# Performance work log

Measured on AMD Instinct MI355X. Metric: run time of the kernel, lower is better.

Reference implementation:

```python
import jax, jax.numpy as jnp
import numpy as np
from jax import lax

VOCAB = 12000
EMB = 512
RNN = 512
FEATS = 4096
SEQ_LEN = 15


def setup_inputs() -> dict:
    key = jax.random.key(0)
    ks = jax.random.split(key, 10)
    B = 1024
    s = 0.05
    return {
        "img_features": jax.random.normal(ks[0], (B, FEATS), jnp.float32),
        "W_feats": jax.random.normal(ks[1], (EMB, FEATS), jnp.float32) * s,
        "b_feats": jax.random.normal(ks[2], (EMB,), jnp.float32) * s,
        "W_ih": jax.random.normal(ks[3], (4 * RNN, EMB), jnp.float32) * s,
        "W_hh": jax.random.normal(ks[4], (4 * RNN, RNN), jnp.float32) * s,
        "b_ih": jax.random.normal(ks[5], (4 * RNN,), jnp.float32) * s,
        "b_hh": jax.random.normal(ks[6], (4 * RNN,), jnp.float32) * s,
        "emb": jax.random.normal(ks[7], (VOCAB, EMB), jnp.float32) * s,
        "W_out": jax.random.normal(ks[8], (VOCAB - 2, RNN), jnp.float32) * s,
        "b_out": jax.random.normal(ks[9], (VOCAB - 2,), jnp.float32) * s,
    }


def reference(img_features, W_feats, b_feats, W_ih, W_hh, b_ih, b_hh, emb, W_out, b_out):
    B = img_features.shape[0]

    def lstm_cell(x, h, c):
        # torch.nn.LSTMCell: gates ordered i, f, g, o
        gates = x @ W_ih.T + b_ih + h @ W_hh.T + b_hh
        i, f, g, o = jnp.split(gates, 4, axis=1)
        c_new = jax.nn.sigmoid(f) * c + jax.nn.sigmoid(i) * jnp.tanh(g)
        h_new = jax.nn.sigmoid(o) * jnp.tanh(c_new)
        return h_new, c_new

    # image feature embedding + ReLU, then prime the LSTM with it
    img_vec = jax.nn.relu(img_features @ W_feats.T + b_feats)  # [B, 512]
    h = jnp.zeros((B, RNN), img_features.dtype)
    c = jnp.zeros((B, RNN), img_features.dtype)
    h, c = lstm_cell(img_vec, h, c)

    def step(carry, _):
        h, c, words = carry
        x = emb[words]                     # [B, 512] embedding lookup
        h, c = lstm_cell(x, h, c)
        logits = h @ W_out.T + b_out       # [B, VOCAB-2]
        idx = jnp.argmax(logits, axis=1).astype(jnp.int32)
        return (h, c, idx + 2), idx

    words0 = jnp.ones((B,), jnp.int32)  # START token = 1
    _, seq = lax.scan(step, (h, c, words0), None, length=SEQ_LEN)
    return seq.T  # [B, SEQ_LEN] greedy-decoded token ids
```

## Files before the change

kernel.cpp:

```cpp
#include <hip/hip_runtime.h>
#include <stdint.h>

#define BATCH  1024
#define SEQLEN 15
#define NGATE  2048
#define NVOCAB 11998
#define FEATS  4096

typedef __attribute__((ext_vector_type(8)))  short  s8v;
typedef __attribute__((ext_vector_type(16))) float  f32x16;
typedef __attribute__((ext_vector_type(8)))  unsigned short us8;

__device__ __forceinline__ unsigned short f2bf(float f) {
    unsigned u = __float_as_uint(f);
    u += 0x7FFFu + ((u >> 16) & 1u);
    return (unsigned short)(u >> 16);
}
__device__ __forceinline__ float bf2f(unsigned short h) {
    return __uint_as_float(((unsigned)h) << 16);
}
struct bfpair { unsigned short hi, lo; };
__device__ __forceinline__ bfpair split2v(float v) {
    bfpair r;
    r.hi = f2bf(v);
    r.lo = f2bf(v - bf2f(r.hi));
    return r;
}
__device__ __forceinline__ void split8(const float* __restrict__ s, us8& vh, us8& vl) {
    #pragma unroll
    for (int e = 0; e < 8; ++e) {
        bfpair q = split2v(s[e]);
        vh[e] = q.hi; vl[e] = q.lo;
    }
}

__device__ __forceinline__ void async_cp16(const void* g, void* l) {
    __builtin_amdgcn_global_load_lds(
        (const __attribute__((address_space(1))) unsigned int*)g,
        (__attribute__((address_space(3))) unsigned int*)l, 16, 0, 0);
}

__global__ void prep_wcat_blk(const float* __restrict__ W_ih, const float* __restrict__ W_hh,
                              const float* __restrict__ b_ih, const float* __restrict__ b_hh,
                              unsigned short* __restrict__ hi, unsigned short* __restrict__ lo,
                              float* __restrict__ bsum) {
    int idx = blockIdx.x * 256 + threadIdx.x;
    int kc = idx >> 11, row = idx & 2047;
    int k = kc << 3;
    const float* src = (k < 512) ? (W_ih + (size_t)row * 512 + k)
                                 : (W_hh + (size_t)row * 512 + (k - 512));
    us8 vh, vl; split8(src, vh, vl);
    *(us8*)(hi + (size_t)idx * 8) = vh;
    *(us8*)(lo + (size_t)idx * 8) = vl;
    if (idx < NGATE) bsum[idx] = b_ih[idx] + b_hh[idx];
}

__global__ void prep_blk(const float* __restrict__ src,
                         unsigned short* __restrict__ hi, unsigned short* __restrict__ lo,
                         int R, int K) {
    int row = blockIdx.x * 256 + threadIdx.x;
    if (row >= R) return;
    int kc = blockIdx.y;
    us8 vh, vl; split8(src + (size_t)row * K + (kc << 3), vh, vl);
    size_t o = ((size_t)kc * R + row) * 8;
    *(us8*)(hi + o) = vh;
    *(us8*)(lo + o) = vl;
}

template<int MODE>
__device__ __forceinline__ void mfma_blk_body(
    const unsigned short* __restrict__ Ahi, const unsigned short* __restrict__ Alo, int aRows,
    const unsigned short* __restrict__ Bhi, const unsigned short* __restrict__ Blo, int bRows,
    const float* __restrict__ bias,
    float* __restrict__ C, int ldc,
    unsigned long long* __restrict__ packed,
    int N, int K, size_t akstride, size_t bkstride, size_t czstride)
{
    __shared__ short smem[4 * 4 * 128 * 8];
    short* sAhi = smem;
    short* sAlo = smem + 4 * 128 * 8;
    short* sBhi = smem + 2 * 4 * 128 * 8;
    short* sBlo = smem + 3 * 4 * 128 * 8;

    const int kz = blockIdx.z;
    Ahi += kz * akstride;  Alo += kz * akstride;
    Bhi += kz * bkstride;  Blo += kz * bkstride;
    if (MODE == 3) C += kz * czstride;

    const int tid  = threadIdx.x;
    const int lane = tid & 63, wave = tid >> 6;
    const int wr = (wave & 1) * 64, wc = (wave >> 1) * 64;
    const int col = lane & 31, kh = lane >> 5;
    const int bm = blockIdx.y * 128, bn = blockIdx.x * 128;

    f32x16 acc[2][2] = {};

    for (int k0 = 0; k0 < K; k0 += 32) {
        const int kc0 = k0 >> 3;
        __syncthreads();
        #pragma unroll
        for (int p = 0; p < 2; ++p) {
            int s    = p * 4 + wave;
            int kc_l = s >> 1, rh = s & 1;
            int rl   = rh * 64 + lane;
            int lo_  = (kc_l * 128 + rh * 64) * 8;
            size_t ga = ((size_t)(kc0 + kc_l) * aRows + (bm + rl)) * 8;
            async_cp16(Ahi + ga, sAhi + lo_);
            async_cp16(Alo + ga, sAlo + lo_);
            int brow = bn + rl; if (brow > N - 1) brow = N - 1;
            size_t gb = ((size_t)(kc0 + kc_l) * bRows + brow) * 8;
            async_cp16(Bhi + gb, sBhi + lo_);
            async_cp16(Blo + gb, sBlo + lo_);
        }
        __syncthreads();

        #pragma unroll
        for (int st = 0; st < 2; ++st) {
            int off = (2 * st + kh) * 128 * 8;
            s8v ah0 = *(const s8v*)(sAhi + off + (wr + col) * 8);
            s8v ah1 = *(const s8v*)(sAhi + off + (wr + 32 + col) * 8);
            s8v al0 = *(const s8v*)(sAlo + off + (wr + col) * 8);
            s8v al1 = *(const s8v*)(sAlo + off + (wr + 32 + col) * 8);
            s8v bh0 = *(const s8v*)(sBhi + off + (wc + col) * 8);
            s8v bh1 = *(const s8v*)(sBhi + off + (wc + 32 + col) * 8);
            s8v bl0 = *(const s8v*)(sBlo + off + (wc + col) * 8);
            s8v bl1 = *(const s8v*)(sBlo + off + (wc + 32 + col) * 8);

            acc[0][0] = __builtin_amdgcn_mfma_f32_32x32x16_bf16(ah0, bh0, acc[0][0], 0, 0, 0);
            acc[0][1] = __builtin_amdgcn_mfma_f32_32x32x16_bf16(ah0, bh1, acc[0][1], 0, 0, 0);
            acc[1][0] = __builtin_amdgcn_mfma_f32_32x32x16_bf16(ah1, bh0, acc[1][0], 0, 0, 0);
            acc[1][1] = __builtin_amdgcn_mfma_f32_32x32x16_bf16(ah1, bh1, acc[1][1], 0, 0, 0);
            acc[0][0] = __builtin_amdgcn_mfma_f32_32x32x16_bf16(ah0, bl0, acc[0][0], 0, 0, 0);
            acc[0][1] = __builtin_amdgcn_mfma_f32_32x32x16_bf16(ah0, bl1, acc[0][1], 0, 0, 0);
            acc[1][0] = __builtin_amdgcn_mfma_f32_32x32x16_bf16(ah1, bl0, acc[1][0], 0, 0, 0);
            acc[1][1] = __builtin_amdgcn_mfma_f32_32x32x16_bf16(ah1, bl1, acc[1][1], 0, 0, 0);
            acc[0][0] = __builtin_amdgcn_mfma_f32_32x32x16_bf16(al0, bh0, acc[0][0], 0, 0, 0);
            acc[0][1] = __builtin_amdgcn_mfma_f32_32x32x16_bf16(al0, bh1, acc[0][1], 0, 0, 0);
            acc[1][0] = __builtin_amdgcn_mfma_f32_32x32x16_bf16(al1, bh0, acc[1][0], 0, 0, 0);
            acc[1][1] = __builtin_amdgcn_mfma_f32_32x32x16_bf16(al1, bh1, acc[1][1], 0, 0, 0);
        }
    }

    if (MODE == 3) {
        #pragma unroll
        for (int i = 0; i < 2; ++i)
            #pragma unroll
            for (int rg = 0; rg < 4; ++rg)
                #pragma unroll
                for (int rr = 0; rr < 4; ++rr) {
                    int reg = rg * 4 + rr;
                    int m = bm + wr + i * 32 + rr + rg * 8 + kh * 4;
                    #pragma unroll
                    for (int j = 0; j < 2; ++j) {
                        int n = bn + wc + j * 32 + col;
                        if (n < N) C[(size_t)m * ldc + n] = acc[i][j][reg];
                    }
                }
    } else {
        #pragma unroll
        for (int i = 0; i < 2; ++i)
            #pragma unroll
            for (int rg = 0; rg < 4; ++rg)
                #pragma unroll
                for (int rr = 0; rr < 4; ++rr) {
                    int reg = rg * 4 + rr;
                    int m = bm + wr + i * 32 + rr + rg * 8 + kh * 4;
                    unsigned long long best = 0ull;
                    #pragma unroll
                    for (int j = 0; j < 2; ++j) {
                        int n = bn + wc + j * 32 + col;
                        if (n < N) {
                            float v = acc[i][j][reg] + bias[n];
                            unsigned int u   = __float_as_uint(v);
                            unsigned int key = (u & 0x80000000u) ? ~u : (u | 0x80000000u);
                            unsigned long long pk =
                                ((unsigned long long)key << 32) |
                                (unsigned long long)(0xFFFFFFFFu - (unsigned)n);
                            best = (pk > best) ? pk : best;
                        }
                    }
                    #pragma unroll
                    for (int sdist = 1; sdist < 32; sdist <<= 1) {
                        unsigned long long o = __shfl_xor(best, sdist, 64);
                        best = (o > best) ? o : best;
                    }
                    if (col == 0) atomicMax(&packed[m], best);
                }
    }
}

__global__ __launch_bounds__(256) void k_gemm_feats(
    const unsigned short* Ahi, const unsigned short* Alo, int aRows,
    const unsigned short* Bhi, const unsigned short* Blo, int bRows,
    float* C, int ldc, int N, int K, size_t aks, size_t bks, size_t czs) {
    mfma_blk_body<3>(Ahi, Alo, aRows, Bhi, Blo, bRows, nullptr, C, ldc, nullptr, N, K, aks, bks, czs);
}
__global__ __launch_bounds__(256) void k_gemm_gates(
    const unsigned short* Ahi, const unsigned short* Alo, int aRows,
    const unsigned short* Bhi, const unsigned short* Blo, int bRows,
    float* C, int ldc, int N, int K, size_t aks, size_t bks, size_t czs) {
    mfma_blk_body<3>(Ahi, Alo, aRows, Bhi, Blo, bRows, nullptr, C, ldc, nullptr, N, K, aks, bks, czs);
}
__global__ __launch_bounds__(256) void k_logits_argmax(
    const unsigned short* Ahi, const unsigned short* Alo, int aRows,
    const unsigned short* Bhi, const unsigned short* Blo, int bRows,
    const float* bias, unsigned long long* packed, int N, int K) {
    mfma_blk_body<2>(Ahi, Alo, aRows, Bhi, Blo, bRows, bias, nullptr, 0, packed, N, K, 0, 0, 0);
}

__global__ void feats_reduce8(const float* __restrict__ part, const float* __restrict__ bias,
                              unsigned short* __restrict__ hi, unsigned short* __restrict__ lo) {
    int idx = blockIdx.x * 256 + threadIdx.x;
    int b = idx >> 6, kc = idx & 63;
    int n = kc << 3;
    float v[8];
    #pragma unroll
    for (int e = 0; e < 8; ++e) v[e] = bias[n + e];
    #pragma unroll
    for (int z = 0; z < 8; ++z) {
        const float* s = part + (size_t)z * 1024 * 512 + (size_t)b * 512 + n;
        #pragma unroll
        for (int e = 0; e < 8; ++e) v[e] += s[e];
    }
    us8 vh, vl;
    #pragma unroll
    for (int e = 0; e < 8; ++e) {
        bfpair q = split2v(fmaxf(v[e], 0.f));
        vh[e] = q.hi; vl[e] = q.lo;
    }
    size_t o = ((size_t)kc * 1024 + b) * 8;
    *(us8*)(hi + o) = vh;
    *(us8*)(lo + o) = vl;
}

template<bool PRIME>
__global__ void lstm_pw_blk(const float* __restrict__ g0, const float* __restrict__ g1,
                            const float* __restrict__ bsum, float* __restrict__ cbuf,
                            unsigned short* __restrict__ xh_hi, unsigned short* __restrict__ xh_lo,
                            unsigned long long* __restrict__ packed) {
    int idx = blockIdx.x * 256 + threadIdx.x;
    int b = idx >> 6, j8 = idx & 63;
    int j = j8 << 3;
    const float* g = g0 + (size_t)b * NGATE;
    float v[4][8];
    #pragma unroll
    for (int gt = 0; gt < 4; ++gt) {
        const float* s = g + gt * 512 + j;
        const float* bs = bsum + gt * 512 + j;
        #pragma unroll
        for (int e = 0; e < 8; ++e) v[gt][e] = s[e] + bs[e];
    }
    if (g1) {
        const float* h2 = g1 + (size_t)b * NGATE;
        #pragma unroll
        for (int gt = 0; gt < 4; ++gt) {
            const float* s = h2 + gt * 512 + j;
            #pragma unroll
            for (int e = 0; e < 8; ++e) v[gt][e] += s[e];
        }
    }
    float* cb = cbuf + (size_t)b * 512 + j;
    us8 vh, vl;
    #pragma unroll
    for (int e = 0; e < 8; ++e) {
        float si = 1.f / (1.f + expf(-v[0][e]));
        float sf = 1.f / (1.f + expf(-v[1][e]));
        float tg = tanhf(v[2][e]);
        float so = 1.f / (1.f + expf(-v[3][e]));
        float cn = PRIME ? (si * tg) : (sf * cb[e] + si * tg);
        cb[e] = cn;
        bfpair q = split2v(so * tanhf(cn));
        vh[e] = q.hi; vl[e] = q.lo;
    }
    size_t o = ((size_t)(64 + j8) * 1024 + b) * 8;
    *(us8*)(xh_hi + o) = vh;
    *(us8*)(xh_lo + o) = vl;
    if (j8 == 0) packed[b] = 0ull;
}

template<int FIRST>
__global__ void gather_blk(const float* __restrict__ emb,
                           const unsigned long long* __restrict__ packed,
                           unsigned short* __restrict__ xh_hi, unsigned short* __restrict__ xh_lo,
                           int* __restrict__ out, int t) {
    int idx = blockIdx.x * 256 + threadIdx.x;
    int b = idx >> 6, kc = idx & 63;
    int word;
    if (FIRST) {
        word = 1;
    } else {
        unsigned long long p = packed[b];
        int id = (int)(0xFFFFFFFFu - (unsigned)(p & 0xFFFFFFFFull));
        word = id + 2;
        if (kc == 0) out[b * SEQLEN + (t - 1)] = id;
    }
    us8 vh, vl; split8(emb + (size_t)word * 512 + (kc << 3), vh, vl);
    size_t o = ((size_t)kc * 1024 + b) * 8;
    *(us8*)(xh_hi + o) = vh;
    *(us8*)(xh_lo + o) = vl;
}

__global__ void final_out(const unsigned long long* __restrict__ packed, int* __restrict__ out) {
    int b = blockIdx.x * 256 + threadIdx.x;
    if (b < BATCH) {
        unsigned long long p = packed[b];
        out[b * SEQLEN + (SEQLEN - 1)] = (int)(0xFFFFFFFFu - (unsigned)(p & 0xFFFFFFFFull));
    }
}

extern "C" void kernel_launch(void* const* d_in, const int* in_sizes, int n_in,
                              void* d_out, int out_size, void* d_ws, size_t ws_size,
                              hipStream_t stream) {
    const float* img     = (const float*)d_in[0];
    const float* W_feats = (const float*)d_in[1];
    const float* b_feats = (const float*)d_in[2];
    const float* W_ih    = (const float*)d_in[3];
    const float* W_hh    = (const float*)d_in[4];
    const float* b_ih    = (const float*)d_in[5];
    const float* b_hh    = (const float*)d_in[6];
    const float* emb     = (const float*)d_in[7];
    const float* W_out   = (const float*)d_in[8];
    const float* b_out   = (const float*)d_in[9];
    int* out = (int*)d_out;

    const size_t WCAT_H = (size_t)128 * 2048 * 8;
    const size_t WOUT_H = (size_t)64 * NVOCAB * 8;
    const size_t XH_H   = (size_t)128 * 1024 * 8;
    const size_t IMGV_H = (size_t)64 * 1024 * 8;

    char* p = (char*)d_ws;
    unsigned short* wcat_hi = (unsigned short*)p;  p += WCAT_H * 2;
    unsigned short* wcat_lo = (unsigned short*)p;  p += WCAT_H * 2;
    unsigned short* wout_hi = (unsigned short*)p;  p += WOUT_H * 2;
    unsigned short* wout_lo = (unsigned short*)p;  p += WOUT_H * 2;
    unsigned short* xh_hi   = (unsigned short*)p;  p += XH_H * 2;
    unsigned short* xh_lo   = (unsigned short*)p;  p += XH_H * 2;
    unsigned short* imgv_hi = (unsigned short*)p;  p += IMGV_H * 2;
    unsigned short* imgv_lo = (unsigned short*)p;  p += IMGV_H * 2;
    float* cbuf             = (float*)p;           p += (size_t)1024 * 512 * 4;
    float* bsum             = (float*)p;           p += (size_t)NGATE * 4;
    unsigned long long* packed = (unsigned long long*)p;  p += (size_t)1024 * 8;
    float* gates0           = (float*)p;           p += (size_t)1024 * NGATE * 4;
    float* gates1           = (float*)p;           p += (size_t)1024 * NGATE * 4;
    unsigned short* imgb_hi = wout_hi;
    unsigned short* imgb_lo = imgb_hi + (size_t)512 * 1024 * 8;
    unsigned short* wfb_hi  = imgb_lo + (size_t)512 * 1024 * 8;
    unsigned short* wfb_lo  = wfb_hi  + (size_t)512 * 512 * 8;
    float* partials = gates0;

    prep_wcat_blk<<<1024, 256, 0, stream>>>(W_ih, W_hh, b_ih, b_hh, wcat_hi, wcat_lo, bsum);
    prep_blk<<<dim3(4, 512), 256, 0, stream>>>(img,     imgb_hi, imgb_lo, 1024, FEATS);
    prep_blk<<<dim3(2, 512), 256, 0, stream>>>(W_feats, wfb_hi,  wfb_lo,  512,  FEATS);

    k_gemm_feats<<<dim3(4, 8, 8), 256, 0, stream>>>(
        imgb_hi, imgb_lo, 1024, wfb_hi, wfb_lo, 512,
        partials, 512, 512, 512,
        (size_t)64 * 1024 * 8, (size_t)64 * 512 * 8, (size_t)1024 * 512);
    feats_reduce8<<<256, 256, 0, stream>>>(partials, b_feats, imgv_hi, imgv_lo);

    prep_blk<<<dim3(47, 64), 256, 0, stream>>>(W_out, wout_hi, wout_lo, NVOCAB, 512);

    k_gemm_gates<<<dim3(16, 8, 1), 256, 0, stream>>>(
        imgv_hi, imgv_lo, 1024, wcat_hi, wcat_lo, 2048,
        gates0, NGATE, NGATE, 512, 0, 0, 0);
    lstm_pw_blk<true><<<256, 256, 0, stream>>>(gates0, nullptr, bsum, cbuf, xh_hi, xh_lo, packed);

    for (int t = 0; t < SEQLEN; ++t) {
        if (t == 0) gather_blk<1><<<256, 256, 0, stream>>>(emb, packed, xh_hi, xh_lo, out, t);
        else        gather_blk<0><<<256, 256, 0, stream>>>(emb, packed, xh_hi, xh_lo, out, t);

        k_gemm_gates<<<dim3(16, 8, 2), 256, 0, stream>>>(
            xh_hi, xh_lo, 1024, wcat_hi, wcat_lo, 2048,
            gates0, NGATE, NGATE, 512,
            (size_t)64 * 1024 * 8, (size_t)64 * 2048 * 8, (size_t)1024 * NGATE);
        lstm_pw_blk<false><<<256, 256, 0, stream>>>(gates0, gates1, bsum, cbuf, xh_hi, xh_lo, packed);

        k_logits_argmax<<<dim3(94, 8, 1), 256, 0, stream>>>(
            xh_hi + (size_t)64 * 1024 * 8, xh_lo + (size_t)64 * 1024 * 8, 1024,
            wout_hi, wout_lo, NVOCAB, b_out, packed, NVOCAB, 512);
    }
    final_out<<<4, 256, 0, stream>>>(packed, out);
}
```

Baseline: 1.845 ms.

## Fuse embedding gather into gates GEMM, double-buffer LDS, swizzle logits blocks by XCD

```diff
diff --git a/kernel.cpp b/kernel.cpp
--- a/kernel.cpp
+++ b/kernel.cpp
@@ -33,6 +33,7 @@
         vh[e] = q.hi; vl[e] = q.lo;
     }
 }
+__device__ __forceinline__ int imin(int a, int b) { return a < b ? a : b; }
 
 __device__ __forceinline__ void async_cp16(const void* g, void* l) {
     __builtin_amdgcn_global_load_lds(
@@ -67,78 +68,121 @@
     *(us8*)(lo + o) = vl;
 }
 
-template<int MODE>
-__device__ __forceinline__ void mfma_blk_body(
+template<int MODE, int AEMB, int FIRST>
+__device__ __forceinline__ void gemm_body(
     const unsigned short* __restrict__ Ahi, const unsigned short* __restrict__ Alo, int aRows,
     const unsigned short* __restrict__ Bhi, const unsigned short* __restrict__ Blo, int bRows,
+    const float* __restrict__ emb, const unsigned long long* __restrict__ packedR,
     const float* __restrict__ bias,
     float* __restrict__ C, int ldc,
     unsigned long long* __restrict__ packed,
-    int N, int K, size_t akstride, size_t bkstride, size_t czstride)
+    int K, size_t akstride, size_t bkstride, size_t czstride,
+    int bm, int bn)
 {
-    __shared__ short smem[4 * 4 * 128 * 8];
-    short* sAhi = smem;
-    short* sAlo = smem + 4 * 128 * 8;
-    short* sBhi = smem + 2 * 4 * 128 * 8;
-    short* sBlo = smem + 3 * 4 * 128 * 8;
-
-    const int kz = blockIdx.z;
-    Ahi += kz * akstride;  Alo += kz * akstride;
-    Bhi += kz * bkstride;  Blo += kz * bkstride;
-    if (MODE == 3) C += kz * czstride;
-
-    const int tid  = threadIdx.x;
+    __shared__ short smem[2 * 8192];
+    const int tid = threadIdx.x;
     const int lane = tid & 63, wave = tid >> 6;
     const int wr = (wave & 1) * 64, wc = (wave >> 1) * 64;
     const int col = lane & 31, kh = lane >> 5;
-    const int bm = blockIdx.y * 128, bn = blockIdx.x * 128;
-
+
+    const int kz = blockIdx.z;
+    Bhi += (size_t)kz * bkstride;  Blo += (size_t)kz * bkstride;
+    const bool embp = AEMB && (kz == 0);
+    if (!embp) { Ahi += (size_t)kz * akstride; Alo += (size_t)kz * akstride; }
+    if (MODE == 3) C += (size_t)kz * czstride;
+
+    const float* embrow = nullptr;
+    int arow = 0, akcp = 0;
+    if (embp) {
+        arow = tid >> 1; akcp = tid & 1;
+        int w = 1;
+        if (!FIRST) {
+            unsigned long long p = packedR[bm + arow];
+            w = (int)(0xFFFFFFFFu - (unsigned)(p & 0xFFFFFFFFull)) + 2;
+        }
+        embrow = emb + (size_t)w * 512 + akcp * 8;
+    }
+
+    const int nIter = K >> 4;
     f32x16 acc[2][2] = {};
 
-    for (int k0 = 0; k0 < K; k0 += 32) {
-        const int kc0 = k0 >> 3;
+    auto stage = [&](int it) {
+        const int kcg = it * 2;
+        short* base = smem + (it & 1) * 8192;
+        if (!embp) {
+            const unsigned short* gsrc = (wave == 0) ? Ahi : (wave == 1) ? Alo
+                                       : (wave == 2) ? Bhi : Blo;
+            const int rows = (wave < 2) ? aRows : bRows;
+            const bool isB = (wave >= 2);
+            short* abase = base + wave * 2048;
+            #pragma unroll
+            for (int p = 0; p < 4; ++p) {
+                int kc_l = p >> 1, rh = p & 1;
+                int rl = rh * 64 + lane;
+                int grow = isB ? imin(bn + rl, rows - 1) : (bm + rl);
+                size_t g = ((size_t)(kcg + kc_l) * rows + grow) * 8;
+                async_cp16(gsrc + g, abase + (kc_l * 128 + rh * 64) * 8);
+            }
+        } else {
+            #pragma unroll
+            for (int p = 0; p < 2; ++p) {
+                int s = wave * 2 + p;
+                int arr = s >> 2, kc_l = (s >> 1) & 1, rh = s & 1;
+                const unsigned short* gsrc = arr ? Blo : Bhi;
+                int rl = rh * 64 + lane;
+                int grow = imin(bn + rl, bRows - 1);
+                size_t g = ((size_t)(kcg + kc_l) * bRows + grow) * 8;
+                async_cp16(gsrc + g, base + (2 + arr) * 2048 + (kc_l * 128 + rh * 64) * 8);
+            }
+            float4 f0 = *(const float4*)(embrow + kcg * 8);
+            float4 f1 = *(const float4*)(embrow + kcg * 8 + 4);
+            float fb[8] = {f0.x, f0.y, f0.z, f0.w, f1.x, f1.y, f1.z, f1.w};
+            us8 vh, vl;
+            #pragma unroll
+            for (int e = 0; e < 8; ++e) {
+                bfpair q = split2v(fb[e]);
+                vh[e] = q.hi; vl[e] = q.lo;
+            }
+            short* d = base + (akcp * 128 + arow) * 8;
+            *(us8*)(d) = vh;
+            *(us8*)(d + 2048) = vl;
+        }
+    };
+
+    auto consume = [&](int it) {
+        short* base = smem + (it & 1) * 8192;
+        const int off = kh * 1024;
+        const short* pAhi = base + off;
+        const short* pAlo = base + 2048 + off;
+        const short* pBhi = base + 4096 + off;
+        const short* pBlo = base + 6144 + off;
+        s8v ah0 = *(const s8v*)(pAhi + (wr + col) * 8);
+        s8v ah1 = *(const s8v*)(pAhi + (wr + 32 + col) * 8);
+        s8v al0 = *(const s8v*)(pAlo + (wr + col) * 8);
+        s8v al1 = *(const s8v*)(pAlo + (wr + 32 + col) * 8);
+        s8v bh0 = *(const s8v*)(pBhi + (wc + col) * 8);
+        s8v bh1 = *(const s8v*)(pBhi + (wc + 32 + col) * 8);
+        s8v bl0 = *(const s8v*)(pBlo + (wc + col) * 8);
+        s8v bl1 = *(const s8v*)(pBlo + (wc + 32 + col) * 8);
+        acc[0][0] = __builtin_amdgcn_mfma_f32_32x32x16_bf16(ah0, bh0, acc[0][0], 0, 0, 0);
+        acc[0][1] = __builtin_amdgcn_mfma_f32_32x32x16_bf16(ah0, bh1, acc[0][1], 0, 0, 0);
+        acc[1][0] = __builtin_amdgcn_mfma_f32_32x32x16_bf16(ah1, bh0, acc[1][0], 0, 0, 0);
+        acc[1][1] = __builtin_amdgcn_mfma_f32_32x32x16_bf16(ah1, bh1, acc[1][1], 0, 0, 0);
+        acc[0][0] = __builtin_amdgcn_mfma_f32_32x32x16_bf16(ah0, bl0, acc[0][0], 0, 0, 0);
+        acc[0][1] = __builtin_amdgcn_mfma_f32_32x32x16_bf16(ah0, bl1, acc[0][1], 0, 0, 0);
+        acc[1][0] = __builtin_amdgcn_mfma_f32_32x32x16_bf16(ah1, bl0, acc[1][0], 0, 0, 0);
+        acc[1][1] = __builtin_amdgcn_mfma_f32_32x32x16_bf16(ah1, bl1, acc[1][1], 0, 0, 0);
+        acc[0][0] = __builtin_amdgcn_mfma_f32_32x32x16_bf16(al0, bh0, acc[0][0], 0, 0, 0);
+        acc[0][1] = __builtin_amdgcn_mfma_f32_32x32x16_bf16(al0, bh1, acc[0][1], 0, 0, 0);
+        acc[1][0] = __builtin_amdgcn_mfma_f32_32x32x16_bf16(al1, bh0, acc[1][0], 0, 0, 0);
+        acc[1][1] = __builtin_amdgcn_mfma_f32_32x32x16_bf16(al1, bh1, acc[1][1], 0, 0, 0);
+    };
+
+    stage(0);
+    for (int it = 0; it < nIter; ++it) {
         __syncthreads();
-        #pragma unroll
-        for (int p = 0; p < 2; ++p) {
-            int s    = p * 4 + wave;
-            int kc_l = s >> 1, rh = s & 1;
-            int rl   = rh * 64 + lane;
-            int lo_  = (kc_l * 128 + rh * 64) * 8;
-            size_t ga = ((size_t)(kc0 + kc_l) * aRows + (bm + rl)) * 8;
-            async_cp16(Ahi + ga, sAhi + lo_);
-            async_cp16(Alo + ga, sAlo + lo_);
-            int brow = bn + rl; if (brow > N - 1) brow = N - 1;
-            size_t gb = ((size_t)(kc0 + kc_l) * bRows + brow) * 8;
-            async_cp16(Bhi + gb, sBhi + lo_);
-            async_cp16(Blo + gb, sBlo + lo_);
-        }
-        __syncthreads();
-
-        #pragma unroll
-        for (int st = 0; st < 2; ++st) {
-            int off = (2 * st + kh) * 128 * 8;
-            s8v ah0 = *(const s8v*)(sAhi + off + (wr + col) * 8);
-            s8v ah1 = *(const s8v*)(sAhi + off + (wr + 32 + col) * 8);
-            s8v al0 = *(const s8v*)(sAlo + off + (wr + col) * 8);
-            s8v al1 = *(const s8v*)(sAlo + off + (wr + 32 + col) * 8);
-            s8v bh0 = *(const s8v*)(sBhi + off + (wc + col) * 8);
-            s8v bh1 = *(const s8v*)(sBhi + off + (wc + 32 + col) * 8);
-            s8v bl0 = *(const s8v*)(sBlo + off + (wc + col) * 8);
-            s8v bl1 = *(const s8v*)(sBlo + off + (wc + 32 + col) * 8);
-
-            acc[0][0] = __builtin_amdgcn_mfma_f32_32x32x16_bf16(ah0, bh0, acc[0][0], 0, 0, 0);
-            acc[0][1] = __builtin_amdgcn_mfma_f32_32x32x16_bf16(ah0, bh1, acc[0][1], 0, 0, 0);
-            acc[1][0] = __builtin_amdgcn_mfma_f32_32x32x16_bf16(ah1, bh0, acc[1][0], 0, 0, 0);
-            acc[1][1] = __builtin_amdgcn_mfma_f32_32x32x16_bf16(ah1, bh1, acc[1][1], 0, 0, 0);
-            acc[0][0] = __builtin_amdgcn_mfma_f32_32x32x16_bf16(ah0, bl0, acc[0][0], 0, 0, 0);
-            acc[0][1] = __builtin_amdgcn_mfma_f32_32x32x16_bf16(ah0, bl1, acc[0][1], 0, 0, 0);
-            acc[1][0] = __builtin_amdgcn_mfma_f32_32x32x16_bf16(ah1, bl0, acc[1][0], 0, 0, 0);
-            acc[1][1] = __builtin_amdgcn_mfma_f32_32x32x16_bf16(ah1, bl1, acc[1][1], 0, 0, 0);
-            acc[0][0] = __builtin_amdgcn_mfma_f32_32x32x16_bf16(al0, bh0, acc[0][0], 0, 0, 0);
-            acc[0][1] = __builtin_amdgcn_mfma_f32_32x32x16_bf16(al0, bh1, acc[0][1], 0, 0, 0);
-            acc[1][0] = __builtin_amdgcn_mfma_f32_32x32x16_bf16(al1, bh0, acc[1][0], 0, 0, 0);
-            acc[1][1] = __builtin_amdgcn_mfma_f32_32x32x16_bf16(al1, bh1, acc[1][1], 0, 0, 0);
-        }
+        if (it + 1 < nIter) stage(it + 1);
+        consume(it);
     }
 
     if (MODE == 3) {
@@ -153,7 +197,7 @@
                     #pragma unroll
                     for (int j = 0; j < 2; ++j) {
                         int n = bn + wc + j * 32 + col;
-                        if (n < N) C[(size_t)m * ldc + n] = acc[i][j][reg];
+                        if (n < bRows) C[(size_t)m * ldc + n] = acc[i][j][reg];
                     }
                 }
     } else {
@@ -169,7 +213,7 @@
                     #pragma unroll
                     for (int j = 0; j < 2; ++j) {
                         int n = bn + wc + j * 32 + col;
-                        if (n < N) {
+                        if (n < bRows) {
                             float v = acc[i][j][reg] + bias[n];
                             unsigned int u   = __float_as_uint(v);
                             unsigned int key = (u & 0x80000000u) ? ~u : (u | 0x80000000u);
@@ -189,23 +233,36 @@
     }
 }
 
-__global__ __launch_bounds__(256) void k_gemm_feats(
+__global__ __launch_bounds__(256) void k_mm(
     const unsigned short* Ahi, const unsigned short* Alo, int aRows,
     const unsigned short* Bhi, const unsigned short* Blo, int bRows,
-    float* C, int ldc, int N, int K, size_t aks, size_t bks, size_t czs) {
-    mfma_blk_body<3>(Ahi, Alo, aRows, Bhi, Blo, bRows, nullptr, C, ldc, nullptr, N, K, aks, bks, czs);
-}
-__global__ __launch_bounds__(256) void k_gemm_gates(
-    const unsigned short* Ahi, const unsigned short* Alo, int aRows,
-    const unsigned short* Bhi, const unsigned short* Blo, int bRows,
-    float* C, int ldc, int N, int K, size_t aks, size_t bks, size_t czs) {
-    mfma_blk_body<3>(Ahi, Alo, aRows, Bhi, Blo, bRows, nullptr, C, ldc, nullptr, N, K, aks, bks, czs);
+    float* C, int ldc, int K, size_t aks, size_t bks, size_t czs) {
+    gemm_body<3, 0, 0>(Ahi, Alo, aRows, Bhi, Blo, bRows, nullptr, nullptr, nullptr,
+                       C, ldc, nullptr, K, aks, bks, czs,
+                       blockIdx.y * 128, blockIdx.x * 128);
+}
+template<int FIRST>
+__global__ __launch_bounds__(256) void k_gates_f(
+    const unsigned short* h_hi, const unsigned short* h_lo,
+    const unsigned short* wcat_hi, const unsigned short* wcat_lo,
+    const float* emb, const unsigned long long* packedR,
+    float* C) {
+    gemm_body<3, 1, FIRST>(h_hi, h_lo, 1024, wcat_hi, wcat_lo, NGATE,
+                           emb, packedR, nullptr, C, NGATE, nullptr,
+                           512, 0, (size_t)64 * NGATE * 8, (size_t)1024 * NGATE,
+                           blockIdx.y * 128, blockIdx.x * 128);
 }
 __global__ __launch_bounds__(256) void k_logits_argmax(
-    const unsigned short* Ahi, const unsigned short* Alo, int aRows,
-    const unsigned short* Bhi, const unsigned short* Blo, int bRows,
-    const float* bias, unsigned long long* packed, int N, int K) {
-    mfma_blk_body<2>(Ahi, Alo, aRows, Bhi, Blo, bRows, bias, nullptr, 0, packed, N, K, 0, 0, 0);
+    const unsigned short* h_hi, const unsigned short* h_lo,
+    const unsigned short* wout_hi, const unsigned short* wout_lo,
+    const float* bias, unsigned long long* packed) {
+    int id = blockIdx.x;
+    int xcd = id & 7, slot = id >> 3;
+    int bn_t = xcd * 12 + (slot % 12);
+    int bm_t = slot / 12;
+    gemm_body<2, 0, 0>(h_hi, h_lo, 1024, wout_hi, wout_lo, NVOCAB,
+                       nullptr, nullptr, bias, nullptr, 0, packed,
+                       512, 0, 0, 0, bm_t * 128, bn_t * 128);
 }
 
 __global__ void feats_reduce8(const float* __restrict__ part, const float* __restrict__ bias,
@@ -236,8 +293,9 @@
 template<bool PRIME>
 __global__ void lstm_pw_blk(const float* __restrict__ g0, const float* __restrict__ g1,
                             const float* __restrict__ bsum, float* __restrict__ cbuf,
-                            unsigned short* __restrict__ xh_hi, unsigned short* __restrict__ xh_lo,
-                            unsigned long long* __restrict__ packed) {
+                            unsigned short* __restrict__ h_hi, unsigned short* __restrict__ h_lo,
+                            unsigned long long* __restrict__ packed,
+                            int* __restrict__ out, int t) {
     int idx = blockIdx.x * 256 + threadIdx.x;
     int b = idx >> 6, j8 = idx & 63;
     int j = j8 << 3;
@@ -272,32 +330,16 @@
         bfpair q = split2v(so * tanhf(cn));
         vh[e] = q.hi; vl[e] = q.lo;
     }
-    size_t o = ((size_t)(64 + j8) * 1024 + b) * 8;
-    *(us8*)(xh_hi + o) = vh;
-    *(us8*)(xh_lo + o) = vl;
-    if (j8 == 0) packed[b] = 0ull;
-}
-
-template<int FIRST>
-__global__ void gather_blk(const float* __restrict__ emb,
-                           const unsigned long long* __restrict__ packed,
-                           unsigned short* __restrict__ xh_hi, unsigned short* __restrict__ xh_lo,
-                           int* __restrict__ out, int t) {
-    int idx = blockIdx.x * 256 + threadIdx.x;
-    int b = idx >> 6, kc = idx & 63;
-    int word;
-    if (FIRST) {
-        word = 1;
-    } else {
-        unsigned long long p = packed[b];
-        int id = (int)(0xFFFFFFFFu - (unsigned)(p & 0xFFFFFFFFull));
-        word = id + 2;
-        if (kc == 0) out[b * SEQLEN + (t - 1)] = id;
-    }
-    us8 vh, vl; split8(emb + (size_t)word * 512 + (kc << 3), vh, vl);
-    size_t o = ((size_t)kc * 1024 + b) * 8;
-    *(us8*)(xh_hi + o) = vh;
-    *(us8*)(xh_lo + o) = vl;
+    size_t o = ((size_t)j8 * 1024 + b) * 8;
+    *(us8*)(h_hi + o) = vh;
+    *(us8*)(h_lo + o) = vl;
+    if (j8 == 0) {
+        if (!PRIME && t > 0) {
+            unsigned long long p = packed[b];
+            out[b * SEQLEN + (t - 1)] = (int)(0xFFFFFFFFu - (unsigned)(p & 0xFFFFFFFFull));
+        }
+        packed[b] = 0ull;
+    }
 }
 
 __global__ void final_out(const unsigned long long* __restrict__ packed, int* __restrict__ out) {
@@ -325,7 +367,7 @@
 
     const size_t WCAT_H = (size_t)128 * 2048 * 8;
     const size_t WOUT_H = (size_t)64 * NVOCAB * 8;
-    const size_t XH_H   = (size_t)128 * 1024 * 8;
+    const size_t H_H    = (size_t)64 * 1024 * 8;
     const size_t IMGV_H = (size_t)64 * 1024 * 8;
 
     char* p = (char*)d_ws;
@@ -333,8 +375,8 @@
     unsigned short* wcat_lo = (unsigned short*)p;  p += WCAT_H * 2;
     unsigned short* wout_hi = (unsigned short*)p;  p += WOUT_H * 2;
     unsigned short* wout_lo = (unsigned short*)p;  p += WOUT_H * 2;
-    unsigned short* xh_hi   = (unsigned short*)p;  p += XH_H * 2;
-    unsigned short* xh_lo   = (unsigned short*)p;  p += XH_H * 2;
+    unsigned short* h_hi    = (unsigned short*)p;  p += H_H * 2;
+    unsigned short* h_lo    = (unsigned short*)p;  p += H_H * 2;
     unsigned short* imgv_hi = (unsigned short*)p;  p += IMGV_H * 2;
     unsigned short* imgv_lo = (unsigned short*)p;  p += IMGV_H * 2;
     float* cbuf             = (float*)p;           p += (size_t)1024 * 512 * 4;
@@ -352,32 +394,30 @@
     prep_blk<<<dim3(4, 512), 256, 0, stream>>>(img,     imgb_hi, imgb_lo, 1024, FEATS);
     prep_blk<<<dim3(2, 512), 256, 0, stream>>>(W_feats, wfb_hi,  wfb_lo,  512,  FEATS);
 
-    k_gemm_feats<<<dim3(4, 8, 8), 256, 0, stream>>>(
+    k_mm<<<dim3(4, 8, 8), 256, 0, stream>>>(
         imgb_hi, imgb_lo, 1024, wfb_hi, wfb_lo, 512,
-        partials, 512, 512, 512,
+        partials, 512, 512,
         (size_t)64 * 1024 * 8, (size_t)64 * 512 * 8, (size_t)1024 * 512);
     feats_reduce8<<<256, 256, 0, stream>>>(partials, b_feats, imgv_hi, imgv_lo);
 
     prep_blk<<<dim3(47, 64), 256, 0, stream>>>(W_out, wout_hi, wout_lo, NVOCAB, 512);
 
-    k_gemm_gates<<<dim3(16, 8, 1), 256, 0, stream>>>(
+    k_mm<<<dim3(16, 8, 1), 256, 0, stream>>>(
         imgv_hi, imgv_lo, 1024, wcat_hi, wcat_lo, 2048,
-        gates0, NGATE, NGATE, 512, 0, 0, 0);
-    lstm_pw_blk<true><<<256, 256, 0, stream>>>(gates0, nullptr, bsum, cbuf, xh_hi, xh_lo, packed);
+        gates0, NGATE, 512, 0, 0, 0);
+    lstm_pw_blk<true><<<256, 256, 0, stream>>>(gates0, nullptr, bsum, cbuf,
+                                               h_hi, h_lo, packed, out, 0);
 
     for (int t = 0; t < SEQLEN; ++t) {
-        if (t == 0) gather_blk<1><<<256, 256, 0, stream>>>(emb, packed, xh_hi, xh_lo, out, t);
-        else        gather_blk<0><<<256, 256, 0, stream>>>(emb, packed, xh_hi, xh_lo, out, t);
-
-        k_gemm_gates<<<dim3(16, 8, 2), 256, 0, stream>>>(
-            xh_hi, xh_lo, 1024, wcat_hi, wcat_lo, 2048,
-            gates0, NGATE, NGATE, 512,
-            (size_t)64 * 1024 * 8, (size_t)64 * 2048 * 8, (size_t)1024 * NGATE);
-        lstm_pw_blk<false><<<256, 256, 0, stream>>>(gates0, gates1, bsum, cbuf, xh_hi, xh_lo, packed);
-
-        k_logits_argmax<<<dim3(94, 8, 1), 256, 0, stream>>>(
-            xh_hi + (size_t)64 * 1024 * 8, xh_lo + (size_t)64 * 1024 * 8, 1024,
-            wout_hi, wout_lo, NVOCAB, b_out, packed, NVOCAB, 512);
+        if (t == 0)
+            k_gates_f<1><<<dim3(16, 8, 2), 256, 0, stream>>>(
+                h_hi, h_lo, wcat_hi, wcat_lo, emb, packed, gates0);
+        else
+            k_gates_f<0><<<dim3(16, 8, 2), 256, 0, stream>>>(
+                h_hi, h_lo, wcat_hi, wcat_lo, emb, packed, gates0);
+        lstm_pw_blk<false><<<256, 256, 0, stream>>>(gates0, gates1, bsum, cbuf,
+                                                    h_hi, h_lo, packed, out, t);
+        k_logits_argmax<<<768, 256, 0, stream>>>(h_hi, h_lo, wout_hi, wout_lo, b_out, packed);
     }
     final_out<<<4, 256, 0, stream>>>(packed, out);
 }
```

Result: slower. 1.948 ms (+5.6%).

## Replace LDS-staged MFMA GEMMs with direct-register flat kernels and drop gates split-K

Applied to the files above, without the earlier changes.

```diff
diff --git a/kernel.cpp b/kernel.cpp
--- a/kernel.cpp
+++ b/kernel.cpp
@@ -32,12 +32,6 @@
         bfpair q = split2v(s[e]);
         vh[e] = q.hi; vl[e] = q.lo;
     }
-}
-
-__device__ __forceinline__ void async_cp16(const void* g, void* l) {
-    __builtin_amdgcn_global_load_lds(
-        (const __attribute__((address_space(1))) unsigned int*)g,
-        (__attribute__((address_space(3))) unsigned int*)l, 16, 0, 0);
 }
 
 __global__ void prep_wcat_blk(const float* __restrict__ W_ih, const float* __restrict__ W_hh,
@@ -67,77 +61,59 @@
     *(us8*)(lo + o) = vl;
 }
 
-template<int MODE>
-__device__ __forceinline__ void mfma_blk_body(
+template<int MODE, int NF, int K>
+__device__ __forceinline__ void flat_body(
     const unsigned short* __restrict__ Ahi, const unsigned short* __restrict__ Alo, int aRows,
     const unsigned short* __restrict__ Bhi, const unsigned short* __restrict__ Blo, int bRows,
-    const float* __restrict__ bias,
-    float* __restrict__ C, int ldc,
+    const float* __restrict__ bias, float* __restrict__ C, int ldc,
     unsigned long long* __restrict__ packed,
-    int N, int K, size_t akstride, size_t bkstride, size_t czstride)
+    int bm, int bn_blk)
 {
-    __shared__ short smem[4 * 4 * 128 * 8];
-    short* sAhi = smem;
-    short* sAlo = smem + 4 * 128 * 8;
-    short* sBhi = smem + 2 * 4 * 128 * 8;
-    short* sBlo = smem + 3 * 4 * 128 * 8;
-
-    const int kz = blockIdx.z;
-    Ahi += kz * akstride;  Alo += kz * akstride;
-    Bhi += kz * bkstride;  Blo += kz * bkstride;
-    if (MODE == 3) C += kz * czstride;
-
-    const int tid  = threadIdx.x;
+    const int tid = threadIdx.x;
     const int lane = tid & 63, wave = tid >> 6;
-    const int wr = (wave & 1) * 64, wc = (wave >> 1) * 64;
     const int col = lane & 31, kh = lane >> 5;
-    const int bm = blockIdx.y * 128, bn = blockIdx.x * 128;
-
-    f32x16 acc[2][2] = {};
-
-    for (int k0 = 0; k0 < K; k0 += 32) {
-        const int kc0 = k0 >> 3;
-        __syncthreads();
-        #pragma unroll
-        for (int p = 0; p < 2; ++p) {
-            int s    = p * 4 + wave;
-            int kc_l = s >> 1, rh = s & 1;
-            int rl   = rh * 64 + lane;
-            int lo_  = (kc_l * 128 + rh * 64) * 8;
-            size_t ga = ((size_t)(kc0 + kc_l) * aRows + (bm + rl)) * 8;
-            async_cp16(Ahi + ga, sAhi + lo_);
-            async_cp16(Alo + ga, sAlo + lo_);
-            int brow = bn + rl; if (brow > N - 1) brow = N - 1;
-            size_t gb = ((size_t)(kc0 + kc_l) * bRows + brow) * 8;
-            async_cp16(Bhi + gb, sBhi + lo_);
-            async_cp16(Blo + gb, sBlo + lo_);
+    const int bn = bn_blk + wave * (NF * 32);
+
+    const size_t aoff = ((size_t)kh * aRows + bm + col) * 8;
+    const unsigned short* pah = Ahi + aoff;
+    const unsigned short* pal = Alo + aoff;
+    const unsigned short* pbh[NF];
+    const unsigned short* pbl[NF];
+    #pragma unroll
+    for (int j = 0; j < NF; ++j) {
+        int br = bn + j * 32 + col;
+        if (br >= bRows) br = bRows - 1;
+        size_t bo = ((size_t)kh * bRows + br) * 8;
+        pbh[j] = Bhi + bo;
+        pbl[j] = Blo + bo;
+    }
+    const size_t astep = (size_t)2 * aRows * 8;
+    const size_t bstep = (size_t)2 * bRows * 8;
+    const int    a32   = 32 * 8;
+
+    f32x16 acc[2][NF] = {};
+    for (int it = 0; it < (K >> 4); ++it) {
+        s8v ah0 = *(const s8v*)(pah);
+        s8v ah1 = *(const s8v*)(pah + a32);
+        s8v al0 = *(const s8v*)(pal);
+        s8v al1 = *(const s8v*)(pal + a32);
+        s8v bh[NF], bl[NF];
+        #pragma unroll
+        for (int j = 0; j < NF; ++j) {
+            bh[j] = *(const s8v*)(pbh[j]);
+            bl[j] = *(const s8v*)(pbl[j]);
         }
-        __syncthreads();
-
-        #pragma unroll
-        for (int st = 0; st < 2; ++st) {
-            int off = (2 * st + kh) * 128 * 8;
-            s8v ah0 = *(const s8v*)(sAhi + off + (wr + col) * 8);
-            s8v ah1 = *(const s8v*)(sAhi + off + (wr + 32 + col) * 8);
-            s8v al0 = *(const s8v*)(sAlo + off + (wr + col) * 8);
-            s8v al1 = *(const s8v*)(sAlo + off + (wr + 32 + col) * 8);
-            s8v bh0 = *(const s8v*)(sBhi + off + (wc + col) * 8);
-            s8v bh1 = *(const s8v*)(sBhi + off + (wc + 32 + col) * 8);
-            s8v bl0 = *(const s8v*)(sBlo + off + (wc + col) * 8);
-            s8v bl1 = *(const s8v*)(sBlo + off + (wc + 32 + col) * 8);
-
-            acc[0][0] = __builtin_amdgcn_mfma_f32_32x32x16_bf16(ah0, bh0, acc[0][0], 0, 0, 0);
-            acc[0][1] = __builtin_amdgcn_mfma_f32_32x32x16_bf16(ah0, bh1, acc[0][1], 0, 0, 0);
-            acc[1][0] = __builtin_amdgcn_mfma_f32_32x32x16_bf16(ah1, bh0, acc[1][0], 0, 0, 0);
-            acc[1][1] = __builtin_amdgcn_mfma_f32_32x32x16_bf16(ah1, bh1, acc[1][1], 0, 0, 0);
-            acc[0][0] = __builtin_amdgcn_mfma_f32_32x32x16_bf16(ah0, bl0, acc[0][0], 0, 0, 0);
-            acc[0][1] = __builtin_amdgcn_mfma_f32_32x32x16_bf16(ah0, bl1, acc[0][1], 0, 0, 0);
-            acc[1][0] = __builtin_amdgcn_mfma_f32_32x32x16_bf16(ah1, bl0, acc[1][0], 0, 0, 0);
-            acc[1][1] = __builtin_amdgcn_mfma_f32_32x32x16_bf16(ah1, bl1, acc[1][1], 0, 0, 0);
-            acc[0][0] = __builtin_amdgcn_mfma_f32_32x32x16_bf16(al0, bh0, acc[0][0], 0, 0, 0);
-            acc[0][1] = __builtin_amdgcn_mfma_f32_32x32x16_bf16(al0, bh1, acc[0][1], 0, 0, 0);
-            acc[1][0] = __builtin_amdgcn_mfma_f32_32x32x16_bf16(al1, bh0, acc[1][0], 0, 0, 0);
-            acc[1][1] = __builtin_amdgcn_mfma_f32_32x32x16_bf16(al1, bh1, acc[1][1], 0, 0, 0);
+        pah += astep; pal += astep;
+        #pragma unroll
+        for (int j = 0; j < NF; ++j) { pbh[j] += bstep; pbl[j] += bstep; }
+        #pragma unroll
+        for (int j = 0; j < NF; ++j) {
+            acc[0][j] = __builtin_amdgcn_mfma_f32_32x32x16_bf16(ah0, bh[j], acc[0][j], 0, 0, 0);
+            acc[1][j] = __builtin_amdgcn_mfma_f32_32x32x16_bf16(ah1, bh[j], acc[1][j], 0, 0, 0);
+            acc[0][j] = __builtin_amdgcn_mfma_f32_32x32x16_bf16(ah0, bl[j], acc[0][j], 0, 0, 0);
+            acc[1][j] = __builtin_amdgcn_mfma_f32_32x32x16_bf16(ah1, bl[j], acc[1][j], 0, 0, 0);
+            acc[0][j] = __builtin_amdgcn_mfma_f32_32x32x16_bf16(al0, bh[j], acc[0][j], 0, 0, 0);
+            acc[1][j] = __builtin_amdgcn_mfma_f32_32x32x16_bf16(al1, bh[j], acc[1][j], 0, 0, 0);
         }
     }
 
@@ -149,11 +125,11 @@
                 #pragma unroll
                 for (int rr = 0; rr < 4; ++rr) {
                     int reg = rg * 4 + rr;
-                    int m = bm + wr + i * 32 + rr + rg * 8 + kh * 4;
+                    int m = bm + i * 32 + rr + rg * 8 + kh * 4;
                     #pragma unroll
-                    for (int j = 0; j < 2; ++j) {
-                        int n = bn + wc + j * 32 + col;
-                        if (n < N) C[(size_t)m * ldc + n] = acc[i][j][reg];
+                    for (int j = 0; j < NF; ++j) {
+                        int n = bn + j * 32 + col;
+                        if (n < bRows) C[(size_t)m * ldc + n] = acc[i][j][reg];
                     }
                 }
     } else {
@@ -164,12 +140,12 @@
                 #pragma unroll
                 for (int rr = 0; rr < 4; ++rr) {
                     int reg = rg * 4 + rr;
-                    int m = bm + wr + i * 32 + rr + rg * 8 + kh * 4;
+                    int m = bm + i * 32 + rr + rg * 8 + kh * 4;
                     unsigned long long best = 0ull;
                     #pragma unroll
-                    for (int j = 0; j < 2; ++j) {
-                        int n = bn + wc + j * 32 + col;
-                        if (n < N) {
+                    for (int j = 0; j < NF; ++j) {
+                        int n = bn + j * 32 + col;
+                        if (n < bRows) {
                             float v = acc[i][j][reg] + bias[n];
                             unsigned int u   = __float_as_uint(v);
                             unsigned int key = (u & 0x80000000u) ? ~u : (u | 0x80000000u);
@@ -189,23 +165,35 @@
     }
 }
 
-__global__ __launch_bounds__(256) void k_gemm_feats(
-    const unsigned short* Ahi, const unsigned short* Alo, int aRows,
-    const unsigned short* Bhi, const unsigned short* Blo, int bRows,
-    float* C, int ldc, int N, int K, size_t aks, size_t bks, size_t czs) {
-    mfma_blk_body<3>(Ahi, Alo, aRows, Bhi, Blo, bRows, nullptr, C, ldc, nullptr, N, K, aks, bks, czs);
-}
-__global__ __launch_bounds__(256) void k_gemm_gates(
-    const unsigned short* Ahi, const unsigned short* Alo, int aRows,
-    const unsigned short* Bhi, const unsigned short* Blo, int bRows,
-    float* C, int ldc, int N, int K, size_t aks, size_t bks, size_t czs) {
-    mfma_blk_body<3>(Ahi, Alo, aRows, Bhi, Blo, bRows, nullptr, C, ldc, nullptr, N, K, aks, bks, czs);
+__global__ __launch_bounds__(256) void k_feats(
+    const unsigned short* Ahi, const unsigned short* Alo,
+    const unsigned short* Bhi, const unsigned short* Blo,
+    float* C) {
+    int kz = blockIdx.z;
+    flat_body<3, 2, 512>(Ahi + (size_t)kz * 64 * 1024 * 8, Alo + (size_t)kz * 64 * 1024 * 8, 1024,
+                         Bhi + (size_t)kz * 64 * 512 * 8,  Blo + (size_t)kz * 64 * 512 * 8,  512,
+                         nullptr, C + (size_t)kz * 1024 * 512, 512, nullptr,
+                         blockIdx.y * 64, blockIdx.x * 256);
+}
+template<int K>
+__global__ __launch_bounds__(256) void k_gates(
+    const unsigned short* Ahi, const unsigned short* Alo,
+    const unsigned short* Bhi, const unsigned short* Blo,
+    float* C) {
+    flat_body<3, 1, K>(Ahi, Alo, 1024, Bhi, Blo, NGATE,
+                       nullptr, C, NGATE, nullptr,
+                       blockIdx.y * 64, blockIdx.x * 128);
 }
 __global__ __launch_bounds__(256) void k_logits_argmax(
-    const unsigned short* Ahi, const unsigned short* Alo, int aRows,
-    const unsigned short* Bhi, const unsigned short* Blo, int bRows,
-    const float* bias, unsigned long long* packed, int N, int K) {
-    mfma_blk_body<2>(Ahi, Alo, aRows, Bhi, Blo, bRows, bias, nullptr, 0, packed, N, K, 0, 0, 0);
+    const unsigned short* h_hi, const unsigned short* h_lo,
+    const unsigned short* wout_hi, const unsigned short* wout_lo,
+    const float* bias, unsigned long long* packed) {
+    int id = blockIdx.x;
+    int xcd = id & 7, slot = id >> 3;
+    int bn_grp = xcd * 6 + (slot % 6);
+    int bm_t = slot / 6;
+    flat_body<2, 2, 512>(h_hi, h_lo, 1024, wout_hi, wout_lo, NVOCAB,
+                         bias, nullptr, 0, packed, bm_t * 64, bn_grp * 256);
 }
 
 __global__ void feats_reduce8(const float* __restrict__ part, const float* __restrict__ bias,
@@ -234,10 +222,11 @@
 }
 
 template<bool PRIME>
-__global__ void lstm_pw_blk(const float* __restrict__ g0, const float* __restrict__ g1,
+__global__ void lstm_pw_blk(const float* __restrict__ g0,
                             const float* __restrict__ bsum, float* __restrict__ cbuf,
                             unsigned short* __restrict__ xh_hi, unsigned short* __restrict__ xh_lo,
-                            unsigned long long* __restrict__ packed) {
+                            unsigned long long* __restrict__ packed,
+                            int* __restrict__ out, int t) {
     int idx = blockIdx.x * 256 + threadIdx.x;
     int b = idx >> 6, j8 = idx & 63;
     int j = j8 << 3;
@@ -249,15 +238,6 @@
         const float* bs = bsum + gt * 512 + j;
         #pragma unroll
         for (int e = 0; e < 8; ++e) v[gt][e] = s[e] + bs[e];
-    }
-    if (g1) {
-        const float* h2 = g1 + (size_t)b * NGATE;
-        #pragma unroll
-        for (int gt = 0; gt < 4; ++gt) {
-            const float* s = h2 + gt * 512 + j;
-            #pragma unroll
-            for (int e = 0; e < 8; ++e) v[gt][e] += s[e];
-        }
     }
     float* cb = cbuf + (size_t)b * 512 + j;
     us8 vh, vl;
@@ -275,24 +255,25 @@
     size_t o = ((size_t)(64 + j8) * 1024 + b) * 8;
     *(us8*)(xh_hi + o) = vh;
     *(us8*)(xh_lo + o) = vl;
-    if (j8 == 0) packed[b] = 0ull;
+    if (j8 == 0) {
+        if (!PRIME && t > 0) {
+            unsigned long long p = packed[b];
+            out[b * SEQLEN + (t - 1)] = (int)(0xFFFFFFFFu - (unsigned)(p & 0xFFFFFFFFull));
+        }
+        packed[b] = 0ull;
+    }
 }
 
 template<int FIRST>
 __global__ void gather_blk(const float* __restrict__ emb,
                            const unsigned long long* __restrict__ packed,
-                           unsigned short* __restrict__ xh_hi, unsigned short* __restrict__ xh_lo,
-                           int* __restrict__ out, int t) {
+                           unsigned short* __restrict__ xh_hi, unsigned short* __restrict__ xh_lo) {
     int idx = blockIdx.x * 256 + threadIdx.x;
     int b = idx >> 6, kc = idx & 63;
-    int word;
-    if (FIRST) {
-        word = 1;
-    } else {
+    int word = 1;
+    if (!FIRST) {
         unsigned long long p = packed[b];
-        int id = (int)(0xFFFFFFFFu - (unsigned)(p & 0xFFFFFFFFull));
-        word = id + 2;
-        if (kc == 0) out[b * SEQLEN + (t - 1)] = id;
+        word = (int)(0xFFFFFFFFu - (unsigned)(p & 0xFFFFFFFFull)) + 2;
     }
     us8 vh, vl; split8(emb + (size_t)word * 512 + (kc << 3), vh, vl);
     size_t o = ((size_t)kc * 1024 + b) * 8;
@@ -352,32 +333,22 @@
     prep_blk<<<dim3(4, 512), 256, 0, stream>>>(img,     imgb_hi, imgb_lo, 1024, FEATS);
     prep_blk<<<dim3(2, 512), 256, 0, stream>>>(W_feats, wfb_hi,  wfb_lo,  512,  FEATS);
 
-    k_gemm_feats<<<dim3(4, 8, 8), 256, 0, stream>>>(
-        imgb_hi, imgb_lo, 1024, wfb_hi, wfb_lo, 512,
-        partials, 512, 512, 512,
-        (size_t)64 * 1024 * 8, (size_t)64 * 512 * 8, (size_t)1024 * 512);
+    k_feats<<<dim3(2, 16, 8), 256, 0, stream>>>(imgb_hi, imgb_lo, wfb_hi, wfb_lo, partials);
     feats_reduce8<<<256, 256, 0, stream>>>(partials, b_feats, imgv_hi, imgv_lo);
 
     prep_blk<<<dim3(47, 64), 256, 0, stream>>>(W_out, wout_hi, wout_lo, NVOCAB, 512);
 
-    k_gemm_gates<<<dim3(16, 8, 1), 256, 0, stream>>>(
-        imgv_hi, imgv_lo, 1024, wcat_hi, wcat_lo, 2048,
-        gates0, NGATE, NGATE, 512, 0, 0, 0);
-    lstm_pw_blk<true><<<256, 256, 0, stream>>>(gates0, nullptr, bsum, cbuf, xh_hi, xh_lo, packed);
+    k_gates<512><<<dim3(16, 16), 256, 0, stream>>>(imgv_hi, imgv_lo, wcat_hi, wcat_lo, gates0);
+    lstm_pw_blk<true><<<256, 256, 0, stream>>>(gates0, bsum, cbuf, xh_hi, xh_lo, packed, out, 0);
 
     for (int t = 0; t < SEQLEN; ++t) {
-        if (t == 0) gather_blk<1><<<256, 256, 0, stream>>>(emb, packed, xh_hi, xh_lo, out, t);
-        else        gather_blk<0><<<256, 256, 0, stream>>>(emb, packed, xh_hi, xh_lo, out, t);
-
-        k_gemm_gates<<<dim3(16, 8, 2), 256, 0, stream>>>(
-            xh_hi, xh_lo, 1024, wcat_hi, wcat_lo, 2048,
-            gates0, NGATE, NGATE, 512,
-            (size_t)64 * 1024 * 8, (size_t)64 * 2048 * 8, (size_t)1024 * NGATE);
-        lstm_pw_blk<false><<<256, 256, 0, stream>>>(gates0, gates1, bsum, cbuf, xh_hi, xh_lo, packed);
-
-        k_logits_argmax<<<dim3(94, 8, 1), 256, 0, stream>>>(
-            xh_hi + (size_t)64 * 1024 * 8, xh_lo + (size_t)64 * 1024 * 8, 1024,
-            wout_hi, wout_lo, NVOCAB, b_out, packed, NVOCAB, 512);
+        if (t == 0) gather_blk<1><<<256, 256, 0, stream>>>(emb, packed, xh_hi, xh_lo);
+        else        gather_blk<0><<<256, 256, 0, stream>>>(emb, packed, xh_hi, xh_lo);
+        k_gates<1024><<<dim3(16, 16), 256, 0, stream>>>(xh_hi, xh_lo, wcat_hi, wcat_lo, gates0);
+        lstm_pw_blk<false><<<256, 256, 0, stream>>>(gates0, bsum, cbuf, xh_hi, xh_lo, packed, out, t);
+        k_logits_argmax<<<768, 256, 0, stream>>>(xh_hi + (size_t)64 * 1024 * 8,
+                                                 xh_lo + (size_t)64 * 1024 * 8,
+                                                 wout_hi, wout_lo, b_out, packed);
     }
     final_out<<<4, 256, 0, stream>>>(packed, out);
 }
```

New measurement: 2.371 ms. +28.5%, slower.
